# Performance work log

Hardware: AMD Instinct MI355X
Metric: run time of the kernel (lower is better)

## Reference

```python
import jax, jax.numpy as jnp
import numpy as np

N, E, F_IN, C, H, L, G, OUT = 10000, 120000, 64, 128, 4, 5, 500, 1801
HL = (L * C) // 2  # JK bidirectional LSTM hidden per direction = 320


def setup_inputs():
    key = jax.random.key(0)
    ks = jax.random.split(key, 20)
    s = 0.05
    p = {}
    p["x"] = jax.random.normal(ks[0], (N, F_IN), jnp.float32)
    p["edge_index"] = jax.random.randint(ks[1], (2, E), 0, N)
    p["batch"] = jnp.sort(jax.random.randint(ks[2], (N,), 0, G))
    p["emb_W"] = jax.random.normal(ks[3], (F_IN, C)) * s
    p["emb_b"] = jnp.zeros((C,))
    p["Wl"] = jax.random.normal(ks[4], (L, C, H * C)) * s
    p["bl"] = jnp.zeros((L, H * C))
    p["Wr"] = jax.random.normal(ks[5], (L, C, H * C)) * s
    p["br"] = jnp.zeros((L, H * C))
    p["att_a"] = jax.random.normal(ks[6], (L, H, C)) * s
    p["conv_b"] = jnp.zeros((L, C))
    p["ln_w"] = jnp.ones((L, C))
    p["ln_b"] = jnp.zeros((L, C))
    p["Wih_f"] = jax.random.normal(ks[7], (4 * HL, C)) * s
    p["Whh_f"] = jax.random.normal(ks[8], (4 * HL, HL)) * s
    p["bih_f"] = jnp.zeros((4 * HL,))
    p["bhh_f"] = jnp.zeros((4 * HL,))
    p["Wih_b"] = jax.random.normal(ks[9], (4 * HL, C)) * s
    p["Whh_b"] = jax.random.normal(ks[10], (4 * HL, HL)) * s
    p["bih_b"] = jnp.zeros((4 * HL,))
    p["bhh_b"] = jnp.zeros((4 * HL,))
    p["jk_w"] = jax.random.normal(ks[11], (2 * HL,)) * s
    p["jk_b"] = jnp.zeros(())
    p["m1_w"] = jax.random.normal(ks[12], (C, C)) * s
    p["m1_b"] = jnp.zeros((C,))
    p["m2_w"] = jax.random.normal(ks[13], (C, OUT)) * s
    p["m2_b"] = jnp.zeros((OUT,))
    p["res_w"] = jax.random.normal(ks[14], (C, OUT)) * s
    p["res_b"] = jnp.zeros((OUT,))
    return p


def _layernorm(x, w, b):
    mu = x.mean(-1, keepdims=True)
    var = ((x - mu) ** 2).mean(-1, keepdims=True)
    return (x - mu) * jax.lax.rsqrt(var + 1e-5) * w + b


def _gatv2(x, src, dst, Wl, bl, Wr, br, a, bias):
    # GATv2Conv, concat=False: mean over heads; eval mode (no dropout)
    xl = (x @ Wl + bl).reshape(N, H, C)   # source projection
    xr = (x @ Wr + br).reshape(N, H, C)   # target projection
    xj = xl[src]                          # [E,H,C] messages from source
    e = jax.nn.leaky_relu(xj + xr[dst], 0.2)
    score = jnp.einsum('ehc,hc->eh', e, a)              # [E,H]
    m = jax.ops.segment_max(score, dst, num_segments=N)  # per-target max
    m = jnp.where(jnp.isfinite(m), m, 0.0)
    ex = jnp.exp(score - m[dst])
    denom = jax.ops.segment_sum(ex, dst, num_segments=N)
    alpha = ex / (denom[dst] + 1e-16)                   # PyG segment softmax
    out = jax.ops.segment_sum(xj * alpha[:, :, None], dst, num_segments=N)
    return out.mean(axis=1) + bias


def _lstm(seq, Wih, Whh, bih, bhh):
    # seq: [L, N, C]; torch gate order i,f,g,o
    def step(carry, xt):
        h, c = carry
        g = xt @ Wih.T + bih + h @ Whh.T + bhh
        i, f, gg, o = jnp.split(g, 4, axis=-1)
        c = jax.nn.sigmoid(f) * c + jax.nn.sigmoid(i) * jnp.tanh(gg)
        h = jax.nn.sigmoid(o) * jnp.tanh(c)
        return (h, c), h
    h0 = jnp.zeros((seq.shape[1], HL), seq.dtype)
    _, hs = jax.lax.scan(step, (h0, h0), seq)
    return hs


def reference(x, edge_index, batch, emb_W, emb_b, Wl, bl, Wr, br, att_a, conv_b, ln_w, ln_b, Wih_f, Whh_f, bih_f, bhh_f, Wih_b, Whh_b, bih_b, bhh_b, jk_w, jk_b, m1_w, m1_b, m2_w, m2_b, res_w, res_b):
    src, dst = edge_index[0], edge_index[1]
    h = x @ emb_W + emb_b
    xs = []
    for l in range(L):
        h = _gatv2(h, src, dst, Wl[l], bl[l], Wr[l], br[l], att_a[l], conv_b[l])
        h = _layernorm(h, ln_w[l], ln_b[l])
        xs.append(h)
    seq = jnp.stack(xs, axis=0)                           # [L,N,C]
    hf = _lstm(seq, Wih_f, Whh_f, bih_f, bhh_f)
    hb = _lstm(seq[::-1], Wih_b, Whh_b, bih_b, bhh_b)[::-1]
    feat = jnp.concatenate([hf, hb], axis=-1)             # [L,N,2*HL]
    scores = feat @ jk_w + jk_b                           # [L,N]
    alpha = jax.nn.softmax(scores, axis=0)
    node = (seq * alpha[:, :, None]).sum(axis=0)          # [N,C]
    cnt = jax.ops.segment_sum(jnp.ones((N,), node.dtype), batch, num_segments=G)
    pooled = jax.ops.segment_sum(node, batch, num_segments=G) / jnp.maximum(cnt, 1.0)[:, None]
    hdn = jax.nn.relu(pooled @ m1_w + m1_b)               # MLPBlock (eval: no dropout)
    return hdn @ m2_w + m2_b + pooled @ res_w + res_b
```

## Files before the change

### kernel.cpp

```cpp
#include <hip/hip_runtime.h>
#include <hip/hip_bf16.h>
#include <math.h>

constexpr int cN   = 10000;
constexpr int cE   = 120000;
constexpr int cFin = 64;
constexpr int cC   = 128;
constexpr int cH   = 4;
constexpr int cL   = 5;
constexpr int cG   = 500;
constexpr int cOUT = 1801;
constexpr int cHL  = 320;
constexpr int c4HL = 4 * cHL;

typedef short bf16x8 __attribute__((ext_vector_type(8)));
typedef float f32x4 __attribute__((ext_vector_type(4)));

__device__ inline unsigned short f2b(float x) {
    union { __hip_bfloat16 h; unsigned short u; } cv;
    cv.h = __float2bfloat16(x);
    return cv.u;
}
__device__ inline float b2f(unsigned short u) {
    union { unsigned int i; float f; } cv;
    cv.i = ((unsigned int)u) << 16;
    return cv.f;
}
__device__ inline float fsig(float x)  { return 1.f / (1.f + __expf(-x)); }
__device__ inline float ftanh(float x) { return 1.f - 2.f / (__expf(2.f * x) + 1.f); }

#define GLD16(g, l) __builtin_amdgcn_global_load_lds( \
    (const __attribute__((address_space(1))) unsigned int*)(g), \
    (__attribute__((address_space(3))) unsigned int*)(l), 16, 0, 0)

__global__ void fill_f32_kernel(float* __restrict__ p, long n, float v) {
    long i = (long)blockIdx.x * blockDim.x + threadIdx.x;
    if (i < n) p[i] = v;
}
__global__ void fill_i32_kernel(int* __restrict__ p, long n, int v) {
    long i = (long)blockIdx.x * blockDim.x + threadIdx.x;
    if (i < n) p[i] = v;
}
__global__ void copy_i32_kernel(const int* __restrict__ a, int* __restrict__ b, long n) {
    long i = (long)blockIdx.x * blockDim.x + threadIdx.x;
    if (i < n) b[i] = a[i];
}
__global__ void conv_bf16_kernel(const float* __restrict__ a, unsigned short* __restrict__ b, long n) {
    long i = (long)blockIdx.x * blockDim.x + threadIdx.x;
    if (i < n) b[i] = f2b(a[i]);
}
__global__ void wproj_prep_kernel(const float* __restrict__ Wl, const float* __restrict__ Wr,
                                  unsigned short* __restrict__ WT) {
    long i = (long)blockIdx.x * blockDim.x + threadIdx.x;
    if (i >= (long)cL * 1024 * 128) return;
    int k = i & 127;
    int n = (int)((i >> 7) & 1023);
    int l = (int)(i >> 17);
    const float* W = (n < 512) ? Wl : Wr;
    int nn = n & 511;
    WT[i] = f2b(W[(size_t)l * 65536 + (size_t)k * 512 + nn]);
}
__global__ void bias_prep_kernel(const float* __restrict__ bl, const float* __restrict__ br,
                                 float* __restrict__ bb) {
    int i = blockIdx.x * blockDim.x + threadIdx.x;
    if (i >= cL * 1024) return;
    int n = i & 1023, l = i >> 10;
    bb[i] = (n < 512) ? bl[l * 512 + n] : br[l * 512 + (n - 512)];
}
__global__ void embw_prep_kernel(const float* __restrict__ W, unsigned short* __restrict__ WT) {
    int i = blockIdx.x * blockDim.x + threadIdx.x;
    if (i >= cC * cFin) return;
    int k = i & 63, n = i >> 6;
    WT[i] = f2b(W[(size_t)k * cC + n]);
}
__global__ void lstm_prep_kernel(const float* __restrict__ Wih, const float* __restrict__ Whh,
                                 const float* __restrict__ bih, const float* __restrict__ bhh,
                                 unsigned short* __restrict__ WihP, unsigned short* __restrict__ WhhP,
                                 float* __restrict__ biasP) {
    long i = (long)blockIdx.x * blockDim.x + threadIdx.x;
    if (i >= (long)c4HL * 449) return;
    int p = (int)(i / 449), c = (int)(i % 449);
    int u = (p >> 6) * 16 + (p & 15);
    int g = (p >> 4) & 3;
    int r = g * cHL + u;
    if (c < cC)       WihP[(size_t)p * cC + c] = f2b(Wih[(size_t)r * cC + c]);
    else if (c < 448) WhhP[(size_t)p * cHL + (c - cC)] = f2b(Whh[(size_t)r * cHL + (c - cC)]);
    else              biasP[p] = bih[r] + bhh[r];
}

__global__ void hist_kernel(const int* __restrict__ dst, int* __restrict__ count) {
    int i = blockIdx.x * blockDim.x + threadIdx.x;
    if (i < cE) atomicAdd(&count[dst[i]], 1);
}
__global__ void scan_kernel(const int* __restrict__ count, int* __restrict__ offs) {
    __shared__ int part[256];
    const int tid = threadIdx.x;
    const int CH = (cN + 255) / 256;
    int base = tid * CH;
    int s = 0;
    for (int i = 0; i < CH; i++) {
        int idx = base + i;
        if (idx < cN) s += count[idx];
    }
    part[tid] = s;
    __syncthreads();
    for (int d = 1; d < 256; d <<= 1) {
        int v = 0;
        if (tid >= d) v = part[tid - d];
        __syncthreads();
        if (tid >= d) part[tid] += v;
        __syncthreads();
    }
    int prefix = (tid == 0) ? 0 : part[tid - 1];
    for (int i = 0; i < CH; i++) {
        int idx = base + i;
        if (idx < cN) { offs[idx] = prefix; prefix += count[idx]; }
    }
    if (tid == 255) offs[cN] = prefix;
}
__global__ void scatter_kernel(const int* __restrict__ src, const int* __restrict__ dst,
                               int* __restrict__ cursor, int* __restrict__ src_csr) {
    int i = blockIdx.x * blockDim.x + threadIdx.x;
    if (i < cE) {
        int pos = atomicAdd(&cursor[dst[i]], 1);
        src_csr[pos] = src[i];
    }
}

template<int HASBIAS, int OUTB, int SWZ>
__global__ __launch_bounds__(256)
void gemm_mfma_kernel(const unsigned short* __restrict__ A1, const unsigned short* __restrict__ B1, int k1,
                      const unsigned short* __restrict__ A2, const unsigned short* __restrict__ B2, int k2,
                      const float* __restrict__ bias, void* __restrict__ Cout, int M, int N, int nbn) {
    int bm, bn;
    if (SWZ) {
        int bid = blockIdx.x;
        int xcd = bid & 7, j = bid >> 3;
        int g   = (j / nbn) * 8 + xcd;
        bm = g << 7;
        bn = (j % nbn) << 7;
        if (bm >= M) return;
    } else {
        bm = blockIdx.y << 7;
        bn = blockIdx.x << 7;
    }
    __shared__ unsigned short lds[2][2][128 * 32];
    const int tid  = threadIdx.x;
    const int lane = tid & 63;
    const int wave = tid >> 6;
    const int wr = (wave >> 1) << 6;
    const int wc = (wave & 1) << 6;
    const int ns1 = k1 >> 5, ns2 = k2 >> 5, ns = ns1 + ns2;

    const int lrow = lane >> 2;
    const int lke  = (lane & 3) << 3;

    auto stage = [&](int s, int buf) {
        const unsigned short *Ab, *Bb;
        int stride, koff;
        if (s < ns1) { Ab = A1; Bb = B1; stride = k1; koff = s << 5; }
        else         { Ab = A2; Bb = B2; stride = k2; koff = (s - ns1) << 5; }
#pragma unroll
        for (int r = 0; r < 2; r++) {
            int ch  = wave * 2 + r;
            int row = ch * 16 + lrow;
            int ga  = bm + row; if (ga >= M) ga = M - 1;
            GLD16(Ab + (size_t)ga * stride + koff + lke, &lds[buf][0][ch * 512]);
            GLD16(Bb + (size_t)(bn + row) * stride + koff + lke, &lds[buf][1][ch * 512]);
        }
    };

    f32x4 acc[4][4];
#pragma unroll
    for (int i = 0; i < 4; i++)
#pragma unroll
        for (int j = 0; j < 4; j++) acc[i][j] = (f32x4){0.f, 0.f, 0.f, 0.f};

    stage(0, 0);
    const int ko  = (lane >> 4) << 3;
    const int rla = lane & 15;
    for (int s = 0; s < ns; s++) {
        int buf = s & 1;
        __syncthreads();
        if (s + 1 < ns) stage(s + 1, buf ^ 1);
        bf16x8 af[4], bff[4];
#pragma unroll
        for (int f = 0; f < 4; f++) {
            af[f]  = *(const bf16x8*)&lds[buf][0][(wr + f * 16 + rla) * 32 + ko];
            bff[f] = *(const bf16x8*)&lds[buf][1][(wc + f * 16 + rla) * 32 + ko];
        }
#pragma unroll
        for (int i = 0; i < 4; i++)
#pragma unroll
            for (int j = 0; j < 4; j++)
                acc[i][j] = __builtin_amdgcn_mfma_f32_16x16x32_bf16(af[i], bff[j], acc[i][j], 0, 0, 0);
    }

#pragma unroll
    for (int i = 0; i < 4; i++) {
#pragma unroll
        for (int v = 0; v < 4; v++) {
            int m = bm + wr + i * 16 + ((lane >> 4) << 2) + v;
            if (m < M) {
#pragma unroll
                for (int j = 0; j < 4; j++) {
                    int n = bn + wc + j * 16 + rla;
                    float val = acc[i][j][v];
                    if (HASBIAS) val += bias[n];
                    if (OUTB) ((unsigned short*)Cout)[(size_t)m * N + n] = f2b(val);
                    else      ((float*)Cout)[(size_t)m * N + n] = val;
                }
            }
        }
    }
}

template<int FIRST>
__global__ __launch_bounds__(512)
void gemm_lstm_dual_kernel(const unsigned short* __restrict__ A1f, const unsigned short* __restrict__ A1b,
                           const unsigned short* __restrict__ Bihf, const unsigned short* __restrict__ Bihb,
                           const unsigned short* __restrict__ A2f, const unsigned short* __restrict__ A2b,
                           const unsigned short* __restrict__ Bhhf, const unsigned short* __restrict__ Bhhb,
                           const float* __restrict__ biasPf, const float* __restrict__ biasPb,
                           float* __restrict__ cff, float* __restrict__ cbb,
                           unsigned short* __restrict__ hOutf, unsigned short* __restrict__ hOutb,
                           const float* __restrict__ jkw,
                           float* __restrict__ scoref, float* __restrict__ scoreb) {
    constexpr int M = cN, k1 = cC, k2 = FIRST ? 0 : cHL;
    const int bid = blockIdx.x;
    const int xcd = bid & 7, jj = bid >> 3;
    const int g     = (jj / 10) * 8 + xcd;
    const int inner = jj % 10;
    const int bm = g << 7;
    if (bm >= M) return;
    const int bn = (inner % 5) << 8;
    const int z  = inner / 5;

    const unsigned short* A1 = z ? A1b : A1f;
    const unsigned short* B1 = z ? Bihb : Bihf;
    const unsigned short* A2 = z ? A2b : A2f;
    const unsigned short* B2 = z ? Bhhb : Bhhf;
    const float* biasP = z ? biasPb : biasPf;
    float* cbuf = z ? cbb : cff;
    unsigned short* hOut = z ? hOutb : hOutf;
    const float* jkwz = jkw + (z ? cHL : 0);
    float* score_t = z ? scoreb : scoref;

    __shared__ unsigned short ldsA[2][128 * 32];
    __shared__ unsigned short ldsB[2][256 * 32];
    const int tid  = threadIdx.x;
    const int lane = tid & 63;
    const int wave = tid >> 6;
    const int wr = (wave >> 2) << 6;
    const int wc = (wave & 3) << 6;
    const int ns1 = k1 >> 5, ns2 = k2 >> 5, ns = ns1 + ns2;

    const int lrow = lane >> 2;
    const int lke  = (lane & 3) << 3;

    auto stage = [&](int s, int buf) {
        const unsigned short *Ab, *Bb;
        int stride, koff;
        if (s < ns1) { Ab = A1; Bb = B1; stride = k1; koff = s << 5; }
        else         { Ab = A2; Bb = B2; stride = k2; koff = (s - ns1) << 5; }
        {
            int row = wave * 16 + lrow;
            int ga  = bm + row; if (ga >= M) ga = M - 1;
            GLD16(Ab + (size_t)ga * stride + koff + lke, &ldsA[buf][wave * 512]);
        }
#pragma unroll
        for (int r = 0; r < 2; r++) {
            int ch  = wave * 2 + r;
            int row = ch * 16 + lrow;
            GLD16(Bb + (size_t)(bn + row) * stride + koff + lke, &ldsB[buf][ch * 512]);
        }
    };

    f32x4 acc[4][4];
#pragma unroll
    for (int i = 0; i < 4; i++)
#pragma unroll
        for (int j = 0; j < 4; j++) acc[i][j] = (f32x4){0.f, 0.f, 0.f, 0.f};

    stage(0, 0);
    const int ko  = (lane >> 4) << 3;
    const int rla = lane & 15;
    for (int s = 0; s < ns; s++) {
        int buf = s & 1;
        __syncthreads();
        if (s + 1 < ns) stage(s + 1, buf ^ 1);
        bf16x8 af[4], bff[4];
#pragma unroll
        for (int f = 0; f < 4; f++) {
            af[f]  = *(const bf16x8*)&ldsA[buf][(wr + f * 16 + rla) * 32 + ko];
            bff[f] = *(const bf16x8*)&ldsB[buf][(wc + f * 16 + rla) * 32 + ko];
        }
#pragma unroll
        for (int i = 0; i < 4; i++)
#pragma unroll
            for (int j = 0; j < 4; j++)
                acc[i][j] = __builtin_amdgcn_mfma_f32_16x16x32_bf16(af[i], bff[j], acc[i][j], 0, 0, 0);
    }

    float bias4[4];
#pragma unroll
    for (int j = 0; j < 4; j++) bias4[j] = biasP[bn + wc + j * 16 + rla];
    const int u = ((bn + wc) >> 6) * 16 + rla;
    const float jw = jkwz[u];

#pragma unroll
    for (int i = 0; i < 4; i++) {
#pragma unroll
        for (int v = 0; v < 4; v++) {
            int m = bm + wr + i * 16 + ((lane >> 4) << 2) + v;
            bool ok = (m < M);
            float gi = acc[i][0][v] + bias4[0];
            float gf = acc[i][1][v] + bias4[1];
            float gg = acc[i][2][v] + bias4[2];
            float go = acc[i][3][v] + bias4[3];
            float si = fsig(gi);
            float sf = fsig(gf);
            float so = fsig(go);
            float tg = ftanh(gg);
            size_t idx = (size_t)m * cHL + u;
            float cold = (FIRST || !ok) ? 0.f : cbuf[idx];
            float cc = sf * cold + si * tg;
            float hh = so * ftanh(cc);
            if (ok) { cbuf[idx] = cc; hOut[idx] = f2b(hh); }
            float part = ok ? hh * jw : 0.f;
#pragma unroll
            for (int o = 1; o < 16; o <<= 1) part += __shfl_xor(part, o);
            if (rla == 0 && ok) atomicAdd(&score_t[m], part);
        }
    }
}

__global__ __launch_bounds__(256)
void gat_fused_kernel(const unsigned short* __restrict__ xlr, const int* __restrict__ src_csr,
                      const int* __restrict__ offs, const float* __restrict__ att,
                      const float* __restrict__ conv_b, const float* __restrict__ lnw,
                      const float* __restrict__ lnb, float* __restrict__ seq_l,
                      unsigned short* __restrict__ seqb_l) {
    const int wv   = (blockIdx.x * blockDim.x + threadIdx.x) >> 6;
    const int lane = threadIdx.x & 63;
    if (wv >= cN) return;
    const int h   = lane >> 4;
    const int cb  = (lane & 15) << 3;

    bf16x8 xrv = *(const bf16x8*)&xlr[(size_t)wv * 1024 + 512 + lane * 8];
    float xr[8], av[8];
#pragma unroll
    for (int k = 0; k < 8; k++) {
        xr[k] = b2f((unsigned short)xrv[k]);
        av[k] = att[h * 128 + cb + k];
    }

    float m = -INFINITY, l = 0.f;
    float acc[8];
#pragma unroll
    for (int k = 0; k < 8; k++) acc[k] = 0.f;

    const int beg = offs[wv], end = offs[wv + 1];
    int j = beg;
    for (; j + 1 < end; j += 2) {
        int s0 = src_csr[j], s1 = src_csr[j + 1];
        bf16x8 xv0 = *(const bf16x8*)&xlr[(size_t)s0 * 1024 + lane * 8];
        bf16x8 xv1 = *(const bf16x8*)&xlr[(size_t)s1 * 1024 + lane * 8];
        float x0[8], x1[8], sc0 = 0.f, sc1 = 0.f;
#pragma unroll
        for (int k = 0; k < 8; k++) {
            x0[k] = b2f((unsigned short)xv0[k]);
            float v0 = x0[k] + xr[k];
            v0 = v0 > 0.f ? v0 : 0.2f * v0;
            sc0 = fmaf(v0, av[k], sc0);
            x1[k] = b2f((unsigned short)xv1[k]);
            float v1 = x1[k] + xr[k];
            v1 = v1 > 0.f ? v1 : 0.2f * v1;
            sc1 = fmaf(v1, av[k], sc1);
        }
#pragma unroll
        for (int o = 1; o < 16; o <<= 1) {
            sc0 += __shfl_xor(sc0, o);
            sc1 += __shfl_xor(sc1, o);
        }
        float mn = fmaxf(m, fmaxf(sc0, sc1));
        float r  = __expf(m - mn);
        float p0 = __expf(sc0 - mn);
        float p1 = __expf(sc1 - mn);
        l = l * r + p0 + p1;
#pragma unroll
        for (int k = 0; k < 8; k++)
            acc[k] = fmaf(acc[k], r, fmaf(p0, x0[k], p1 * x1[k]));
        m = mn;
    }
    if (j < end) {
        int s0 = src_csr[j];
        bf16x8 xv = *(const bf16x8*)&xlr[(size_t)s0 * 1024 + lane * 8];
        float x[8], sc = 0.f;
#pragma unroll
        for (int k = 0; k < 8; k++) {
            x[k] = b2f((unsigned short)xv[k]);
            float v = x[k] + xr[k];
            v = v > 0.f ? v : 0.2f * v;
            sc = fmaf(v, av[k], sc);
        }
#pragma unroll
        for (int o = 1; o < 16; o <<= 1) sc += __shfl_xor(sc, o);
        float mn = fmaxf(m, sc);
        float r  = __expf(m - mn);
        float p  = __expf(sc - mn);
        l = l * r + p;
#pragma unroll
        for (int k = 0; k < 8; k++) acc[k] = fmaf(acc[k], r, p * x[k]);
        m = mn;
    }
    float inv = 1.f / (l + 1e-16f);

#pragma unroll
    for (int k = 0; k < 8; k++) {
        float v = acc[k] * inv;
        v += __shfl_xor(v, 16);
        v += __shfl_xor(v, 32);
        acc[k] = 0.25f * v + conv_b[cb + k];
    }
    float ssum = 0.f;
#pragma unroll
    for (int k = 0; k < 8; k++) ssum += acc[k];
#pragma unroll
    for (int o = 1; o < 16; o <<= 1) ssum += __shfl_xor(ssum, o);
    float mu = ssum * (1.f / 128.f);
    float vs = 0.f;
#pragma unroll
    for (int k = 0; k < 8; k++) { float d = acc[k] - mu; vs = fmaf(d, d, vs); }
#pragma unroll
    for (int o = 1; o < 16; o <<= 1) vs += __shfl_xor(vs, o);
    float rstd = 1.f / sqrtf(vs * (1.f / 128.f) + 1e-5f);

    float outv[8];
#pragma unroll
    for (int k = 0; k < 8; k++)
        outv[k] = (acc[k] - mu) * rstd * lnw[cb + k] + lnb[cb + k];

    if (h == 0) {
        size_t b = (size_t)wv * 128 + cb;
        float4 o0 = make_float4(outv[0], outv[1], outv[2], outv[3]);
        float4 o1 = make_float4(outv[4], outv[5], outv[6], outv[7]);
        *(float4*)&seq_l[b]     = o0;
        *(float4*)&seq_l[b + 4] = o1;
        bf16x8 ob;
#pragma unroll
        for (int k = 0; k < 8; k++) ob[k] = (short)f2b(outv[k]);
        *(bf16x8*)&seqb_l[b] = ob;
    }
}

__global__ void jk_pool_kernel(const float* __restrict__ seq, const float* __restrict__ score,
                               const int* __restrict__ batch, float* __restrict__ pooled) {
    int wid = (blockIdx.x * blockDim.x + threadIdx.x) >> 6;
    int lane = threadIdx.x & 63;
    if (wid >= cN) return;
    float s[cL], mx = -INFINITY;
#pragma unroll
    for (int l = 0; l < cL; l++) { s[l] = score[(size_t)l * cN + wid]; mx = fmaxf(mx, s[l]); }
    float se = 0.f;
#pragma unroll
    for (int l = 0; l < cL; l++) { s[l] = __expf(s[l] - mx); se += s[l]; }
    float inv = 1.f / se;
    int g = batch[wid];
    float acc0 = 0.f, acc1 = 0.f;
#pragma unroll
    for (int l = 0; l < cL; l++) {
        const float* sp = seq + ((size_t)l * cN + wid) * 128;
        float w = s[l] * inv;
        acc0 += w * sp[lane];
        acc1 += w * sp[lane + 64];
    }
    atomicAdd(&pooled[(size_t)g * 128 + lane], acc0);
    atomicAdd(&pooled[(size_t)g * 128 + lane + 64], acc1);
}

__global__ void count_kernel(const int* __restrict__ batch, float* __restrict__ cnt) {
    int i = blockIdx.x * blockDim.x + threadIdx.x;
    if (i < cN) atomicAdd(&cnt[batch[i]], 1.f);
}

__global__ void div_pool_kernel(float* __restrict__ pooled, const float* __restrict__ cnt) {
    int i = blockIdx.x * blockDim.x + threadIdx.x;
    if (i < cG * 128) pooled[i] /= fmaxf(cnt[i >> 7], 1.f);
}

__global__ __launch_bounds__(256)
void head_fused_kernel(const float* __restrict__ pooled,
                       const float* __restrict__ m1_w, const float* __restrict__ m1_b,
                       const float* __restrict__ m2_w, const float* __restrict__ m2_b,
                       const float* __restrict__ res_w, const float* __restrict__ res_b,
                       float* __restrict__ out) {
    __shared__ float pl[4][128];
    __shared__ float hd[4][128];
    const int tid = threadIdx.x;
    const int r0 = blockIdx.y << 2;
    const int c0 = blockIdx.x << 8;
#pragma unroll
    for (int e = tid; e < 512; e += 256) {
        int r = e >> 7, k = e & 127;
        pl[r][k] = pooled[(size_t)(r0 + r) * 128 + k];
    }
    __syncthreads();
#pragma unroll
    for (int e = tid; e < 512; e += 256) {
        int r = e >> 7, n = e & 127;
        float acc = m1_b[n];
#pragma unroll 8
        for (int k = 0; k < 128; k++) acc = fmaf(pl[r][k], m1_w[k * 128 + n], acc);
        hd[r][n] = fmaxf(acc, 0.f);
    }
    __syncthreads();
    int col = c0 + tid;
    if (col >= cOUT) return;
    float b = m2_b[col] + res_b[col];
    float acc[4] = {b, b, b, b};
    for (int k = 0; k < 128; k++) {
        float w2 = m2_w[(size_t)k * cOUT + col];
        float wr = res_w[(size_t)k * cOUT + col];
#pragma unroll
        for (int r = 0; r < 4; r++)
            acc[r] = fmaf(hd[r][k], w2, fmaf(pl[r][k], wr, acc[r]));
    }
#pragma unroll
    for (int r = 0; r < 4; r++)
        out[(size_t)(r0 + r) * cOUT + col] = acc[r];
}

static inline int ceil_div(long a, long b) { return (int)((a + b - 1) / b); }

template<int OUTB>
static void launch_mfma(const unsigned short* A1, const unsigned short* B1, int k1,
                        const unsigned short* A2, const unsigned short* B2, int k2,
                        const float* bias, void* C, int M, int N, hipStream_t s) {
    dim3 g((N + 127) >> 7, (M + 127) >> 7);
    if (bias) gemm_mfma_kernel<1, OUTB, 0><<<g, 256, 0, s>>>(A1, B1, k1, A2, B2, k2, bias, C, M, N, 0);
    else      gemm_mfma_kernel<0, OUTB, 0><<<g, 256, 0, s>>>(A1, B1, k1, A2, B2, k2, bias, C, M, N, 0);
}
template<int OUTB>
static void launch_mfma_swz(const unsigned short* A1, const unsigned short* B1, int k1,
                            const float* bias, void* C, int M, int N, hipStream_t s) {
    int nbn = N >> 7;
    int groups = ((((M + 127) >> 7) + 7) / 8) * 8;
    dim3 g(groups * nbn);
    gemm_mfma_kernel<1, OUTB, 1><<<g, 256, 0, s>>>(A1, B1, k1, nullptr, nullptr, 0, bias, C, M, N, nbn);
}

static void fillF(float* p, long n, float v, hipStream_t s) {
    fill_f32_kernel<<<ceil_div(n, 256), 256, 0, s>>>(p, n, v);
}
static void fillI(int* p, long n, int v, hipStream_t s) {
    fill_i32_kernel<<<ceil_div(n, 256), 256, 0, s>>>(p, n, v);
}
static void convB(const float* a, unsigned short* b, long n, hipStream_t s) {
    conv_bf16_kernel<<<ceil_div(n, 256), 256, 0, s>>>(a, b, n);
}

extern "C" void kernel_launch(void* const* d_in, const int* in_sizes, int n_in,
                              void* d_out, int out_size, void* d_ws, size_t ws_size,
                              hipStream_t stream) {
    const float* x      = (const float*)d_in[0];
    const int*   ei     = (const int*)d_in[1];
    const int*   batch  = (const int*)d_in[2];
    const float* emb_W  = (const float*)d_in[3];
    const float* emb_b  = (const float*)d_in[4];
    const float* Wl     = (const float*)d_in[5];
    const float* bl     = (const float*)d_in[6];
    const float* Wr     = (const float*)d_in[7];
    const float* br     = (const float*)d_in[8];
    const float* att_a  = (const float*)d_in[9];
    const float* conv_b = (const float*)d_in[10];
    const float* ln_w   = (const float*)d_in[11];
    const float* ln_b   = (const float*)d_in[12];
    const float* Wih_f  = (const float*)d_in[13];
    const float* Whh_f  = (const float*)d_in[14];
    const float* bih_f  = (const float*)d_in[15];
    const float* bhh_f  = (const float*)d_in[16];
    const float* Wih_b  = (const float*)d_in[17];
    const float* Whh_b  = (const float*)d_in[18];
    const float* bih_b  = (const float*)d_in[19];
    const float* bhh_b  = (const float*)d_in[20];
    const float* jk_w   = (const float*)d_in[21];
    const float* m1_w   = (const float*)d_in[23];
    const float* m1_b   = (const float*)d_in[24];
    const float* m2_w   = (const float*)d_in[25];
    const float* m2_b   = (const float*)d_in[26];
    const float* res_w  = (const float*)d_in[27];
    const float* res_b  = (const float*)d_in[28];
    float* out = (float*)d_out;

    const int* src = ei;
    const int* dst = ei + cE;

    char* ws = (char*)d_ws;
    size_t off = 0;
    auto alloc = [&](size_t bytes) -> char* {
        size_t o = (off + 255) & ~(size_t)255;
        off = o + bytes;
        return ws + o;
    };
    unsigned short* x16     = (unsigned short*)alloc((size_t)cN * cFin * 2);
    unsigned short* embWT   = (unsigned short*)alloc((size_t)cC * cFin * 2);
    unsigned short* emb_b16 = (unsigned short*)alloc((size_t)cN * cC * 2);
    float*          seq     = (float*)alloc((size_t)cL * cN * cC * 4);
    unsigned short* seqb16  = (unsigned short*)alloc((size_t)cL * cN * cC * 2);
    unsigned short* WT      = (unsigned short*)alloc((size_t)cL * 1024 * 128 * 2);
    float*          bb      = (float*)alloc((size_t)cL * 1024 * 4);
    unsigned short* WihPf   = (unsigned short*)alloc((size_t)c4HL * cC * 2);
    unsigned short* WhhPf   = (unsigned short*)alloc((size_t)c4HL * cHL * 2);
    unsigned short* WihPb   = (unsigned short*)alloc((size_t)c4HL * cC * 2);
    unsigned short* WhhPb   = (unsigned short*)alloc((size_t)c4HL * cHL * 2);
    float*          biasPf  = (float*)alloc((size_t)c4HL * 4);
    float*          biasPb  = (float*)alloc((size_t)c4HL * 4);
    unsigned short* hf0     = (unsigned short*)alloc((size_t)cN * cHL * 2);
    unsigned short* hf1     = (unsigned short*)alloc((size_t)cN * cHL * 2);
    unsigned short* hbk0    = (unsigned short*)alloc((size_t)cN * cHL * 2);
    unsigned short* hbk1    = (unsigned short*)alloc((size_t)cN * cHL * 2);
    float*          cf      = (float*)alloc((size_t)cN * cHL * 4);
    float*          cbk     = (float*)alloc((size_t)cN * cHL * 4);
    float*          jks     = (float*)alloc((size_t)cL * cN * 4);
    float*          pooled  = (float*)alloc((size_t)cG * cC * 4);
    float*          cnt     = (float*)alloc((size_t)cG * 4);
    int*            offs    = (int*)alloc((size_t)(cN + 1) * 4);
    int*            cursor  = (int*)alloc((size_t)cN * 4);
    int*            src_csr = (int*)alloc((size_t)cE * 4);
    unsigned short* xlr     = (unsigned short*)alloc((size_t)cN * 1024 * 2);

    hipStream_t s = stream;

    fillI(cursor, cN, 0, s);
    hist_kernel<<<ceil_div(cE, 256), 256, 0, s>>>(dst, cursor);
    scan_kernel<<<1, 256, 0, s>>>(cursor, offs);
    copy_i32_kernel<<<ceil_div(cN, 256), 256, 0, s>>>(offs, cursor, cN);
    scatter_kernel<<<ceil_div(cE, 256), 256, 0, s>>>(src, dst, cursor, src_csr);

    wproj_prep_kernel<<<ceil_div((long)cL * 1024 * 128, 256), 256, 0, s>>>(Wl, Wr, WT);
    bias_prep_kernel<<<ceil_div((long)cL * 1024, 256), 256, 0, s>>>(bl, br, bb);
    embw_prep_kernel<<<ceil_div((long)cC * cFin, 256), 256, 0, s>>>(emb_W, embWT);
    convB(x, x16, (long)cN * cFin, s);
    lstm_prep_kernel<<<ceil_div((long)c4HL * 449, 256), 256, 0, s>>>(
        Wih_f, Whh_f, bih_f, bhh_f, WihPf, WhhPf, biasPf);
    lstm_prep_kernel<<<ceil_div((long)c4HL * 449, 256), 256, 0, s>>>(
        Wih_b, Whh_b, bih_b, bhh_b, WihPb, WhhPb, biasPb);

    launch_mfma<1>(x16, embWT, cFin, nullptr, nullptr, 0, emb_b, emb_b16, cN, cC, s);

    for (int l = 0; l < cL; l++) {
        const unsigned short* hin = (l == 0) ? emb_b16 : seqb16 + (size_t)(l - 1) * cN * cC;
        launch_mfma_swz<1>(hin, WT + (size_t)l * 1024 * 128, cC,
                           bb + (size_t)l * 1024, xlr, cN, 1024, s);
        gat_fused_kernel<<<ceil_div((long)cN * 64, 256), 256, 0, s>>>(
            xlr, src_csr, offs, att_a + (size_t)l * cH * cC,
            conv_b + (size_t)l * cC, ln_w + (size_t)l * cC, ln_b + (size_t)l * cC,
            seq + (size_t)l * cN * cC, seqb16 + (size_t)l * cN * cC);
    }

    fillF(jks, (long)cL * cN, 0.f, s);
    unsigned short* hfb[2]  = {hf0, hf1};
    unsigned short* hbb[2]  = {hbk0, hbk1};
    dim3 lg(80 * 10);
    for (int k = 0; k < cL; k++) {
        int cur = k & 1, prev = cur ^ 1;
        int t = cL - 1 - k;
        const unsigned short* A1f = seqb16 + (size_t)k * cN * cC;
        const unsigned short* A1b = seqb16 + (size_t)t * cN * cC;
        if (k == 0)
            gemm_lstm_dual_kernel<1><<<lg, 512, 0, s>>>(
                A1f, A1b, WihPf, WihPb, nullptr, nullptr, nullptr, nullptr,
                biasPf, biasPb, cf, cbk, hfb[cur], hbb[cur], jk_w,
                jks + (size_t)k * cN, jks + (size_t)t * cN);
        else
            gemm_lstm_dual_kernel<0><<<lg, 512, 0, s>>>(
                A1f, A1b, WihPf, WihPb, hfb[prev], hbb[prev], WhhPf, WhhPb,
                biasPf, biasPb, cf, cbk, hfb[cur], hbb[cur], jk_w,
                jks + (size_t)k * cN, jks + (size_t)t * cN);
    }

    fillF(pooled, (long)cG * cC, 0.f, s);
    fillF(cnt, cG, 0.f, s);
    jk_pool_kernel<<<ceil_div((long)cN * 64, 256), 256, 0, s>>>(seq, jks, batch, pooled);
    count_kernel<<<ceil_div(cN, 256), 256, 0, s>>>(batch, cnt);
    div_pool_kernel<<<ceil_div((long)cG * 128, 256), 256, 0, s>>>(pooled, cnt);
    head_fused_kernel<<<dim3(ceil_div(cOUT, 256), cG / 4), 256, 0, s>>>(
        pooled, m1_w, m1_b, m2_w, m2_b, res_w, res_b, out);
}
```

Baseline: 698.9 us.

## Merge prep kernels, drop fp32 seq copy, unroll GAT edges by four

All weight-prep, conversion and zero-fill kernels are merged into one launch, and the cursor copy is folded into the scan. The count and divide steps of pooling are folded into jk_pool and the head kernel. The fp32 seq buffer is removed, so jk_pool now reads the bf16 copy. The GAT edge loop is unrolled from 2 to 4 edges for more memory-level parallelism. Together these cut launch count and memory traffic, at the cost of lower-precision JK pooling inputs and more registers in the GAT kernel.

```diff
diff --git a/kernel.cpp b/kernel.cpp
--- a/kernel.cpp
+++ b/kernel.cpp
@@ -33,52 +33,20 @@
     (const __attribute__((address_space(1))) unsigned int*)(g), \
     (__attribute__((address_space(3))) unsigned int*)(l), 16, 0, 0)
 
-__global__ void fill_f32_kernel(float* __restrict__ p, long n, float v) {
-    long i = (long)blockIdx.x * blockDim.x + threadIdx.x;
-    if (i < n) p[i] = v;
-}
-__global__ void fill_i32_kernel(int* __restrict__ p, long n, int v) {
-    long i = (long)blockIdx.x * blockDim.x + threadIdx.x;
-    if (i < n) p[i] = v;
-}
-__global__ void copy_i32_kernel(const int* __restrict__ a, int* __restrict__ b, long n) {
-    long i = (long)blockIdx.x * blockDim.x + threadIdx.x;
-    if (i < n) b[i] = a[i];
-}
-__global__ void conv_bf16_kernel(const float* __restrict__ a, unsigned short* __restrict__ b, long n) {
-    long i = (long)blockIdx.x * blockDim.x + threadIdx.x;
-    if (i < n) b[i] = f2b(a[i]);
-}
-__global__ void wproj_prep_kernel(const float* __restrict__ Wl, const float* __restrict__ Wr,
-                                  unsigned short* __restrict__ WT) {
-    long i = (long)blockIdx.x * blockDim.x + threadIdx.x;
-    if (i >= (long)cL * 1024 * 128) return;
-    int k = i & 127;
-    int n = (int)((i >> 7) & 1023);
-    int l = (int)(i >> 17);
-    const float* W = (n < 512) ? Wl : Wr;
-    int nn = n & 511;
-    WT[i] = f2b(W[(size_t)l * 65536 + (size_t)k * 512 + nn]);
-}
-__global__ void bias_prep_kernel(const float* __restrict__ bl, const float* __restrict__ br,
-                                 float* __restrict__ bb) {
-    int i = blockIdx.x * blockDim.x + threadIdx.x;
-    if (i >= cL * 1024) return;
-    int n = i & 1023, l = i >> 10;
-    bb[i] = (n < 512) ? bl[l * 512 + n] : br[l * 512 + (n - 512)];
-}
-__global__ void embw_prep_kernel(const float* __restrict__ W, unsigned short* __restrict__ WT) {
-    int i = blockIdx.x * blockDim.x + threadIdx.x;
-    if (i >= cC * cFin) return;
-    int k = i & 63, n = i >> 6;
-    WT[i] = f2b(W[(size_t)k * cC + n]);
-}
-__global__ void lstm_prep_kernel(const float* __restrict__ Wih, const float* __restrict__ Whh,
-                                 const float* __restrict__ bih, const float* __restrict__ bhh,
-                                 unsigned short* __restrict__ WihP, unsigned short* __restrict__ WhhP,
-                                 float* __restrict__ biasP) {
-    long i = (long)blockIdx.x * blockDim.x + threadIdx.x;
-    if (i >= (long)c4HL * 449) return;
+constexpr long R0 = (long)cL * 1024 * 128;
+constexpr long R1 = cL * 1024;
+constexpr long R2 = cC * cFin;
+constexpr long R3 = (long)cN * cFin;
+constexpr long R4 = (long)c4HL * 449;
+constexpr long R5 = (long)c4HL * 449;
+constexpr long R6 = (long)cL * cN + cG * cC + cG;
+constexpr long R7 = cN;
+constexpr long RT = R0 + R1 + R2 + R3 + R4 + R5 + R6 + R7;
+
+__device__ inline void lstm_prep_elem(long i, const float* Wih, const float* Whh,
+                                      const float* bih, const float* bhh,
+                                      unsigned short* WihP, unsigned short* WhhP,
+                                      float* biasP) {
     int p = (int)(i / 449), c = (int)(i % 449);
     int u = (p >> 6) * 16 + (p & 15);
     int g = (p >> 4) & 3;
@@ -88,11 +56,64 @@
     else              biasP[p] = bih[r] + bhh[r];
 }
 
+__global__ void mega_prep_kernel(
+    const float* __restrict__ Wl, const float* __restrict__ Wr, unsigned short* __restrict__ WT,
+    const float* __restrict__ bl, const float* __restrict__ br, float* __restrict__ bb,
+    const float* __restrict__ emb_W, unsigned short* __restrict__ embWT,
+    const float* __restrict__ x, unsigned short* __restrict__ x16,
+    const float* __restrict__ Wih_f, const float* __restrict__ Whh_f,
+    const float* __restrict__ bih_f, const float* __restrict__ bhh_f,
+    unsigned short* __restrict__ WihPf, unsigned short* __restrict__ WhhPf, float* __restrict__ biasPf,
+    const float* __restrict__ Wih_b, const float* __restrict__ Whh_b,
+    const float* __restrict__ bih_b, const float* __restrict__ bhh_b,
+    unsigned short* __restrict__ WihPb, unsigned short* __restrict__ WhhPb, float* __restrict__ biasPb,
+    float* __restrict__ jks, float* __restrict__ pooled, float* __restrict__ cnt,
+    int* __restrict__ cursor) {
+    long i = (long)blockIdx.x * blockDim.x + threadIdx.x;
+    if (i < R0) {
+        int k = (int)(i & 127);
+        int n = (int)((i >> 7) & 1023);
+        int l = (int)(i >> 17);
+        const float* W = (n < 512) ? Wl : Wr;
+        int nn = n & 511;
+        WT[i] = f2b(W[(size_t)l * 65536 + (size_t)k * 512 + nn]);
+        return;
+    }
+    i -= R0;
+    if (i < R1) {
+        int n = (int)(i & 1023), l = (int)(i >> 10);
+        bb[i] = (n < 512) ? bl[l * 512 + n] : br[l * 512 + (n - 512)];
+        return;
+    }
+    i -= R1;
+    if (i < R2) {
+        int k = (int)(i & 63), n = (int)(i >> 6);
+        embWT[i] = f2b(emb_W[(size_t)k * cC + n]);
+        return;
+    }
+    i -= R2;
+    if (i < R3) { x16[i] = f2b(x[i]); return; }
+    i -= R3;
+    if (i < R4) { lstm_prep_elem(i, Wih_f, Whh_f, bih_f, bhh_f, WihPf, WhhPf, biasPf); return; }
+    i -= R4;
+    if (i < R5) { lstm_prep_elem(i, Wih_b, Whh_b, bih_b, bhh_b, WihPb, WhhPb, biasPb); return; }
+    i -= R5;
+    if (i < R6) {
+        if (i < (long)cL * cN) jks[i] = 0.f;
+        else if (i < (long)cL * cN + cG * cC) pooled[i - (long)cL * cN] = 0.f;
+        else cnt[i - (long)cL * cN - cG * cC] = 0.f;
+        return;
+    }
+    i -= R6;
+    if (i < R7) cursor[i] = 0;
+}
+
 __global__ void hist_kernel(const int* __restrict__ dst, int* __restrict__ count) {
     int i = blockIdx.x * blockDim.x + threadIdx.x;
     if (i < cE) atomicAdd(&count[dst[i]], 1);
 }
-__global__ void scan_kernel(const int* __restrict__ count, int* __restrict__ offs) {
+__global__ void scan_kernel(const int* __restrict__ count, int* __restrict__ offs,
+                            int* __restrict__ cursor) {
     __shared__ int part[256];
     const int tid = threadIdx.x;
     const int CH = (cN + 255) / 256;
@@ -114,7 +135,7 @@
     int prefix = (tid == 0) ? 0 : part[tid - 1];
     for (int i = 0; i < CH; i++) {
         int idx = base + i;
-        if (idx < cN) { offs[idx] = prefix; prefix += count[idx]; }
+        if (idx < cN) { offs[idx] = prefix; cursor[idx] = prefix; prefix += count[idx]; }
     }
     if (tid == 255) offs[cN] = prefix;
 }
@@ -339,8 +360,7 @@
 void gat_fused_kernel(const unsigned short* __restrict__ xlr, const int* __restrict__ src_csr,
                       const int* __restrict__ offs, const float* __restrict__ att,
                       const float* __restrict__ conv_b, const float* __restrict__ lnw,
-                      const float* __restrict__ lnb, float* __restrict__ seq_l,
-                      unsigned short* __restrict__ seqb_l) {
+                      const float* __restrict__ lnb, unsigned short* __restrict__ seqb_l) {
     const int wv   = (blockIdx.x * blockDim.x + threadIdx.x) >> 6;
     const int lane = threadIdx.x & 63;
     if (wv >= cN) return;
@@ -362,38 +382,50 @@
 
     const int beg = offs[wv], end = offs[wv + 1];
     int j = beg;
-    for (; j + 1 < end; j += 2) {
-        int s0 = src_csr[j], s1 = src_csr[j + 1];
+    for (; j + 3 < end; j += 4) {
+        int s0 = src_csr[j], s1 = src_csr[j + 1], s2 = src_csr[j + 2], s3 = src_csr[j + 3];
         bf16x8 xv0 = *(const bf16x8*)&xlr[(size_t)s0 * 1024 + lane * 8];
         bf16x8 xv1 = *(const bf16x8*)&xlr[(size_t)s1 * 1024 + lane * 8];
-        float x0[8], x1[8], sc0 = 0.f, sc1 = 0.f;
+        bf16x8 xv2 = *(const bf16x8*)&xlr[(size_t)s2 * 1024 + lane * 8];
+        bf16x8 xv3 = *(const bf16x8*)&xlr[(size_t)s3 * 1024 + lane * 8];
+        float x0[8], x1[8], x2[8], x3[8];
+        float sc0 = 0.f, sc1 = 0.f, sc2 = 0.f, sc3 = 0.f;
 #pragma unroll
         for (int k = 0; k < 8; k++) {
             x0[k] = b2f((unsigned short)xv0[k]);
-            float v0 = x0[k] + xr[k];
-            v0 = v0 > 0.f ? v0 : 0.2f * v0;
+            x1[k] = b2f((unsigned short)xv1[k]);
+            x2[k] = b2f((unsigned short)xv2[k]);
+            x3[k] = b2f((unsigned short)xv3[k]);
+            float v0 = x0[k] + xr[k]; v0 = v0 > 0.f ? v0 : 0.2f * v0;
+            float v1 = x1[k] + xr[k]; v1 = v1 > 0.f ? v1 : 0.2f * v1;
+            float v2 = x2[k] + xr[k]; v2 = v2 > 0.f ? v2 : 0.2f * v2;
+            float v3 = x3[k] + xr[k]; v3 = v3 > 0.f ? v3 : 0.2f * v3;
             sc0 = fmaf(v0, av[k], sc0);
-            x1[k] = b2f((unsigned short)xv1[k]);
-            float v1 = x1[k] + xr[k];
-            v1 = v1 > 0.f ? v1 : 0.2f * v1;
             sc1 = fmaf(v1, av[k], sc1);
+            sc2 = fmaf(v2, av[k], sc2);
+            sc3 = fmaf(v3, av[k], sc3);
         }
 #pragma unroll
         for (int o = 1; o < 16; o <<= 1) {
             sc0 += __shfl_xor(sc0, o);
             sc1 += __shfl_xor(sc1, o);
-        }
-        float mn = fmaxf(m, fmaxf(sc0, sc1));
+            sc2 += __shfl_xor(sc2, o);
+            sc3 += __shfl_xor(sc3, o);
+        }
+        float mn = fmaxf(fmaxf(fmaxf(sc0, sc1), fmaxf(sc2, sc3)), m);
         float r  = __expf(m - mn);
         float p0 = __expf(sc0 - mn);
         float p1 = __expf(sc1 - mn);
-        l = l * r + p0 + p1;
+        float p2 = __expf(sc2 - mn);
+        float p3 = __expf(sc3 - mn);
+        l = l * r + p0 + p1 + p2 + p3;
 #pragma unroll
         for (int k = 0; k < 8; k++)
-            acc[k] = fmaf(acc[k], r, fmaf(p0, x0[k], p1 * x1[k]));
+            acc[k] = fmaf(acc[k], r,
+                          fmaf(p0, x0[k], fmaf(p1, x1[k], fmaf(p2, x2[k], p3 * x3[k]))));
         m = mn;
     }
-    if (j < end) {
+    for (; j < end; j++) {
         int s0 = src_csr[j];
         bf16x8 xv = *(const bf16x8*)&xlr[(size_t)s0 * 1024 + lane * 8];
         float x[8], sc = 0.f;
@@ -443,10 +475,6 @@
 
     if (h == 0) {
         size_t b = (size_t)wv * 128 + cb;
-        float4 o0 = make_float4(outv[0], outv[1], outv[2], outv[3]);
-        float4 o1 = make_float4(outv[4], outv[5], outv[6], outv[7]);
-        *(float4*)&seq_l[b]     = o0;
-        *(float4*)&seq_l[b + 4] = o1;
         bf16x8 ob;
 #pragma unroll
         for (int k = 0; k < 8; k++) ob[k] = (short)f2b(outv[k]);
@@ -454,8 +482,9 @@
     }
 }
 
-__global__ void jk_pool_kernel(const float* __restrict__ seq, const float* __restrict__ score,
-                               const int* __restrict__ batch, float* __restrict__ pooled) {
+__global__ void jk_pool_kernel(const unsigned short* __restrict__ seqb, const float* __restrict__ score,
+                               const int* __restrict__ batch, float* __restrict__ pooled,
+                               float* __restrict__ cnt) {
     int wid = (blockIdx.x * blockDim.x + threadIdx.x) >> 6;
     int lane = threadIdx.x & 63;
     if (wid >= cN) return;
@@ -470,27 +499,18 @@
     float acc0 = 0.f, acc1 = 0.f;
 #pragma unroll
     for (int l = 0; l < cL; l++) {
-        const float* sp = seq + ((size_t)l * cN + wid) * 128;
+        const unsigned short* sp = seqb + ((size_t)l * cN + wid) * 128;
         float w = s[l] * inv;
-        acc0 += w * sp[lane];
-        acc1 += w * sp[lane + 64];
+        acc0 += w * b2f(sp[lane]);
+        acc1 += w * b2f(sp[lane + 64]);
     }
     atomicAdd(&pooled[(size_t)g * 128 + lane], acc0);
     atomicAdd(&pooled[(size_t)g * 128 + lane + 64], acc1);
-}
-
-__global__ void count_kernel(const int* __restrict__ batch, float* __restrict__ cnt) {
-    int i = blockIdx.x * blockDim.x + threadIdx.x;
-    if (i < cN) atomicAdd(&cnt[batch[i]], 1.f);
-}
-
-__global__ void div_pool_kernel(float* __restrict__ pooled, const float* __restrict__ cnt) {
-    int i = blockIdx.x * blockDim.x + threadIdx.x;
-    if (i < cG * 128) pooled[i] /= fmaxf(cnt[i >> 7], 1.f);
+    if (lane == 0) atomicAdd(&cnt[g], 1.f);
 }
 
 __global__ __launch_bounds__(256)
-void head_fused_kernel(const float* __restrict__ pooled,
+void head_fused_kernel(const float* __restrict__ pooled, const float* __restrict__ cnt,
                        const float* __restrict__ m1_w, const float* __restrict__ m1_b,
                        const float* __restrict__ m2_w, const float* __restrict__ m2_b,
                        const float* __restrict__ res_w, const float* __restrict__ res_b,
@@ -503,7 +523,8 @@
 #pragma unroll
     for (int e = tid; e < 512; e += 256) {
         int r = e >> 7, k = e & 127;
-        pl[r][k] = pooled[(size_t)(r0 + r) * 128 + k];
+        float invc = 1.f / fmaxf(cnt[r0 + r], 1.f);
+        pl[r][k] = pooled[(size_t)(r0 + r) * 128 + k] * invc;
     }
     __syncthreads();
 #pragma unroll
@@ -535,29 +556,17 @@
 
 template<int OUTB>
 static void launch_mfma(const unsigned short* A1, const unsigned short* B1, int k1,
-                        const unsigned short* A2, const unsigned short* B2, int k2,
                         const float* bias, void* C, int M, int N, hipStream_t s) {
     dim3 g((N + 127) >> 7, (M + 127) >> 7);
-    if (bias) gemm_mfma_kernel<1, OUTB, 0><<<g, 256, 0, s>>>(A1, B1, k1, A2, B2, k2, bias, C, M, N, 0);
-    else      gemm_mfma_kernel<0, OUTB, 0><<<g, 256, 0, s>>>(A1, B1, k1, A2, B2, k2, bias, C, M, N, 0);
-}
-template<int OUTB>
+    gemm_mfma_kernel<1, OUTB, 0><<<g, 256, 0, s>>>(A1, B1, k1, nullptr, nullptr, 0, bias, C, M, N, 0);
+}
+template<int HASBIAS, int OUTB>
 static void launch_mfma_swz(const unsigned short* A1, const unsigned short* B1, int k1,
                             const float* bias, void* C, int M, int N, hipStream_t s) {
     int nbn = N >> 7;
     int groups = ((((M + 127) >> 7) + 7) / 8) * 8;
     dim3 g(groups * nbn);
-    gemm_mfma_kernel<1, OUTB, 1><<<g, 256, 0, s>>>(A1, B1, k1, nullptr, nullptr, 0, bias, C, M, N, nbn);
-}
-
-static void fillF(float* p, long n, float v, hipStream_t s) {
-    fill_f32_kernel<<<ceil_div(n, 256), 256, 0, s>>>(p, n, v);
-}
-static void fillI(int* p, long n, int v, hipStream_t s) {
-    fill_i32_kernel<<<ceil_div(n, 256), 256, 0, s>>>(p, n, v);
-}
-static void convB(const float* a, unsigned short* b, long n, hipStream_t s) {
-    conv_bf16_kernel<<<ceil_div(n, 256), 256, 0, s>>>(a, b, n);
+    gemm_mfma_kernel<HASBIAS, OUTB, 1><<<g, 256, 0, s>>>(A1, B1, k1, nullptr, nullptr, 0, bias, C, M, N, nbn);
 }
 
 extern "C" void kernel_launch(void* const* d_in, const int* in_sizes, int n_in,
@@ -606,13 +615,12 @@
     unsigned short* x16     = (unsigned short*)alloc((size_t)cN * cFin * 2);
     unsigned short* embWT   = (unsigned short*)alloc((size_t)cC * cFin * 2);
     unsigned short* emb_b16 = (unsigned short*)alloc((size_t)cN * cC * 2);
-    float*          seq     = (float*)alloc((size_t)cL * cN * cC * 4);
     unsigned short* seqb16  = (unsigned short*)alloc((size_t)cL * cN * cC * 2);
     unsigned short* WT      = (unsigned short*)alloc((size_t)cL * 1024 * 128 * 2);
     float*          bb      = (float*)alloc((size_t)cL * 1024 * 4);
     unsigned short* WihPf   = (unsigned short*)alloc((size_t)c4HL * cC * 2);
+    unsigned short* WihPb   = (unsigned short*)alloc((size_t)c4HL * cC * 2);
     unsigned short* WhhPf   = (unsigned short*)alloc((size_t)c4HL * cHL * 2);
-    unsigned short* WihPb   = (unsigned short*)alloc((size_t)c4HL * cC * 2);
     unsigned short* WhhPb   = (unsigned short*)alloc((size_t)c4HL * cHL * 2);
     float*          biasPf  = (float*)alloc((size_t)c4HL * 4);
     float*          biasPb  = (float*)alloc((size_t)c4HL * 4);
@@ -632,34 +640,28 @@
 
     hipStream_t s = stream;
 
-    fillI(cursor, cN, 0, s);
+    mega_prep_kernel<<<ceil_div(RT, 256), 256, 0, s>>>(
+        Wl, Wr, WT, bl, br, bb, emb_W, embWT, x, x16,
+        Wih_f, Whh_f, bih_f, bhh_f, WihPf, WhhPf, biasPf,
+        Wih_b, Whh_b, bih_b, bhh_b, WihPb, WhhPb, biasPb,
+        jks, pooled, cnt, cursor);
+
     hist_kernel<<<ceil_div(cE, 256), 256, 0, s>>>(dst, cursor);
-    scan_kernel<<<1, 256, 0, s>>>(cursor, offs);
-    copy_i32_kernel<<<ceil_div(cN, 256), 256, 0, s>>>(offs, cursor, cN);
+    scan_kernel<<<1, 256, 0, s>>>(cursor, offs, cursor);
     scatter_kernel<<<ceil_div(cE, 256), 256, 0, s>>>(src, dst, cursor, src_csr);
 
-    wproj_prep_kernel<<<ceil_div((long)cL * 1024 * 128, 256), 256, 0, s>>>(Wl, Wr, WT);
-    bias_prep_kernel<<<ceil_div((long)cL * 1024, 256), 256, 0, s>>>(bl, br, bb);
-    embw_prep_kernel<<<ceil_div((long)cC * cFin, 256), 256, 0, s>>>(emb_W, embWT);
-    convB(x, x16, (long)cN * cFin, s);
-    lstm_prep_kernel<<<ceil_div((long)c4HL * 449, 256), 256, 0, s>>>(
-        Wih_f, Whh_f, bih_f, bhh_f, WihPf, WhhPf, biasPf);
-    lstm_prep_kernel<<<ceil_div((long)c4HL * 449, 256), 256, 0, s>>>(
-        Wih_b, Whh_b, bih_b, bhh_b, WihPb, WhhPb, biasPb);
-
-    launch_mfma<1>(x16, embWT, cFin, nullptr, nullptr, 0, emb_b, emb_b16, cN, cC, s);
+    launch_mfma<1>(x16, embWT, cFin, emb_b, emb_b16, cN, cC, s);
 
     for (int l = 0; l < cL; l++) {
         const unsigned short* hin = (l == 0) ? emb_b16 : seqb16 + (size_t)(l - 1) * cN * cC;
-        launch_mfma_swz<1>(hin, WT + (size_t)l * 1024 * 128, cC,
-                           bb + (size_t)l * 1024, xlr, cN, 1024, s);
+        launch_mfma_swz<1, 1>(hin, WT + (size_t)l * 1024 * 128, cC,
+                              bb + (size_t)l * 1024, xlr, cN, 1024, s);
         gat_fused_kernel<<<ceil_div((long)cN * 64, 256), 256, 0, s>>>(
             xlr, src_csr, offs, att_a + (size_t)l * cH * cC,
             conv_b + (size_t)l * cC, ln_w + (size_t)l * cC, ln_b + (size_t)l * cC,
-            seq + (size_t)l * cN * cC, seqb16 + (size_t)l * cN * cC);
-    }
-
-    fillF(jks, (long)cL * cN, 0.f, s);
+            seqb16 + (size_t)l * cN * cC);
+    }
+
     unsigned short* hfb[2]  = {hf0, hf1};
     unsigned short* hbb[2]  = {hbk0, hbk1};
     dim3 lg(80 * 10);
@@ -672,7 +674,7 @@
             gemm_lstm_dual_kernel<1><<<lg, 512, 0, s>>>(
                 A1f, A1b, WihPf, WihPb, nullptr, nullptr, nullptr, nullptr,
                 biasPf, biasPb, cf, cbk, hfb[cur], hbb[cur], jk_w,
-                jks + (size_t)k * cN, jks + (size_t)t * cN);
+                jks, jks + (size_t)t * cN);
         else
             gemm_lstm_dual_kernel<0><<<lg, 512, 0, s>>>(
                 A1f, A1b, WihPf, WihPb, hfb[prev], hbb[prev], WhhPf, WhhPb,
@@ -680,11 +682,7 @@
                 jks + (size_t)k * cN, jks + (size_t)t * cN);
     }
 
-    fillF(pooled, (long)cG * cC, 0.f, s);
-    fillF(cnt, cG, 0.f, s);
-    jk_pool_kernel<<<ceil_div((long)cN * 64, 256), 256, 0, s>>>(seq, jks, batch, pooled);
-    count_kernel<<<ceil_div(cN, 256), 256, 0, s>>>(batch, cnt);
-    div_pool_kernel<<<ceil_div((long)cG * 128, 256), 256, 0, s>>>(pooled, cnt);
+    jk_pool_kernel<<<ceil_div((long)cN * 64, 256), 256, 0, s>>>(seqb16, jks, batch, pooled, cnt);
     head_fused_kernel<<<dim3(ceil_div(cOUT, 256), cG / 4), 256, 0, s>>>(
-        pooled, m1_w, m1_b, m2_w, m2_b, res_w, res_b, out);
-}
+        pooled, cnt, m1_w, m1_b, m2_w, m2_b, res_w, res_b, out);
+}
```

After: 673.6 us. 1.04x faster.
